# Performance work log

Measured on AMD Instinct MI355X. Metric: run time of the kernel, lower is better.

The kernel has to match this reference:

```python
import jax, jax.numpy as jnp
import numpy as np
import math

M, DIN, DTGT = 65536, 256, 256   # feature count and feature dims
S, SD_IN, SD_TGT = 64, 256, 256  # num_slots, in_slot_dim, tgt_slot_dim
ITERS = 3
H_IN = 128                        # mlp_in hidden (hardcoded 128 in source)
H_TGT = SD_TGT if SD_TGT > 128 else 128  # mlp_tgt hidden

ARGS = ["inputs", "target", "in_slots", "tgt_slots",
        "ln_in_g", "ln_in_b", "ln_tgt_g", "ln_tgt_b",
        "Wk", "bk", "Wv", "bv", "Wvt", "bvt",
        "ln_slots_g", "ln_slots_b", "Wq", "bq",
        "gru_in_Wih", "gru_in_Whh", "gru_in_bih", "gru_in_bhh",
        "gru_tgt_Wih", "gru_tgt_Whh", "gru_tgt_bih", "gru_tgt_bhh",
        "ln_mi_g", "ln_mi_b", "mi_W1", "mi_b1", "mi_W2", "mi_b2",
        "ln_mt_g", "ln_mt_b", "mt_W1", "mt_b1", "mt_W2", "mt_b2"]


def _ln(x, g, b):
    m = jnp.mean(x, axis=-1, keepdims=True)
    v = jnp.var(x, axis=-1, keepdims=True)
    return (x - m) * jax.lax.rsqrt(v + 1e-5) * g + b


def _gru(x, h, Wih, Whh, bih, bhh):
    # torch.nn.GRUCell semantics; Wih: (D, 3H), Whh: (H, 3H)
    H = h.shape[-1]
    gi = x @ Wih + bih
    gh = h @ Whh + bhh
    r = jax.nn.sigmoid(gi[:, :H] + gh[:, :H])
    z = jax.nn.sigmoid(gi[:, H:2 * H] + gh[:, H:2 * H])
    n = jnp.tanh(gi[:, 2 * H:] + r * gh[:, 2 * H:])
    return (1.0 - z) * n + z * h


def _forward(inputs, target, in_slots, tgt_slots,
             ln_in_g, ln_in_b, ln_tgt_g, ln_tgt_b,
             Wk, bk, Wv, bv, Wvt, bvt,
             ln_slots_g, ln_slots_b, Wq, bq,
             gru_in_Wih, gru_in_Whh, gru_in_bih, gru_in_bhh,
             gru_tgt_Wih, gru_tgt_Whh, gru_tgt_bih, gru_tgt_bhh,
             ln_mi_g, ln_mi_b, mi_W1, mi_b1, mi_W2, mi_b2,
             ln_mt_g, ln_mt_b, mt_W1, mt_b1, mt_W2, mt_b2):
    inputs_norm = _ln(inputs, ln_in_g, ln_in_b)          # [M, DIN]
    in_k = inputs_norm @ Wk + bk                          # [M, SD_IN]
    in_v = inputs_norm @ Wv + bv                          # [M, SD_IN]
    tgt_v = _ln(target, ln_tgt_g, ln_tgt_b) @ Wvt + bvt   # [M, SD_TGT]
    scale = 1.0 / math.sqrt(in_k.shape[1])
    attn = None
    for _ in range(ITERS):
        q = _ln(in_slots, ln_slots_g, ln_slots_b) @ Wq + bq   # [S, SD_IN]
        logits = (q @ in_k.T) * scale                          # [S, M]
        attn = jax.nn.softmax(logits, axis=0)                  # softmax over SLOTS (dim=0)
        in_up = attn @ in_v                                    # [S, SD_IN]
        tgt_up = attn @ tgt_v                                  # [S, SD_TGT]
        in_slots = _gru(in_up, in_slots, gru_in_Wih, gru_in_Whh, gru_in_bih, gru_in_bhh)
        tgt_slots = _gru(tgt_up, tgt_slots, gru_tgt_Wih, gru_tgt_Whh, gru_tgt_bih, gru_tgt_bhh)
        in_slots = in_slots + (jax.nn.relu(_ln(in_slots, ln_mi_g, ln_mi_b) @ mi_W1 + mi_b1) @ mi_W2 + mi_b2)
        tgt_slots = tgt_slots + (jax.nn.relu(_ln(tgt_slots, ln_mt_g, ln_mt_b) @ mt_W1 + mt_b1) @ mt_W2 + mt_b2)
    return (in_slots, tgt_slots, attn)


def setup_inputs() -> dict:
    key = jax.random.key(0)
    ks = iter(jax.random.split(key, 64))
    rn = lambda shape, s=1.0: jax.random.normal(next(ks), shape, dtype=jnp.float32) * s
    w = 0.02
    d = {
        "inputs": rn((M, DIN)),
        "target": rn((M, DTGT)),
        "in_slots": rn((S, SD_IN)),
        "tgt_slots": rn((S, SD_TGT)),
        "ln_in_g": jnp.ones((DIN,)), "ln_in_b": jnp.zeros((DIN,)),
        "ln_tgt_g": jnp.ones((DTGT,)), "ln_tgt_b": jnp.zeros((DTGT,)),
        "Wk": rn((DIN, SD_IN), w), "bk": jnp.zeros((SD_IN,)),
        "Wv": rn((DIN, SD_IN), w), "bv": jnp.zeros((SD_IN,)),
        "Wvt": rn((DTGT, SD_TGT), w), "bvt": jnp.zeros((SD_TGT,)),
        "ln_slots_g": jnp.ones((SD_IN,)), "ln_slots_b": jnp.zeros((SD_IN,)),
        "Wq": rn((SD_IN, SD_IN), w), "bq": jnp.zeros((SD_IN,)),
        "gru_in_Wih": rn((SD_IN, 3 * SD_IN), w), "gru_in_Whh": rn((SD_IN, 3 * SD_IN), w),
        "gru_in_bih": jnp.zeros((3 * SD_IN,)), "gru_in_bhh": jnp.zeros((3 * SD_IN,)),
        "gru_tgt_Wih": rn((SD_TGT, 3 * SD_TGT), w), "gru_tgt_Whh": rn((SD_TGT, 3 * SD_TGT), w),
        "gru_tgt_bih": jnp.zeros((3 * SD_TGT,)), "gru_tgt_bhh": jnp.zeros((3 * SD_TGT,)),
        "ln_mi_g": jnp.ones((SD_IN,)), "ln_mi_b": jnp.zeros((SD_IN,)),
        "mi_W1": rn((SD_IN, H_IN), w), "mi_b1": jnp.zeros((H_IN,)),
        "mi_W2": rn((H_IN, SD_IN), w), "mi_b2": jnp.zeros((SD_IN,)),
        "ln_mt_g": jnp.ones((SD_TGT,)), "ln_mt_b": jnp.zeros((SD_TGT,)),
        "mt_W1": rn((SD_TGT, H_TGT), w), "mt_b1": jnp.zeros((H_TGT,)),
        "mt_W2": rn((H_TGT, SD_TGT), w), "mt_b2": jnp.zeros((SD_TGT,)),
    }
    return {k: d[k] for k in ARGS}


def reference(inputs, target, in_slots, tgt_slots,
              ln_in_g, ln_in_b, ln_tgt_g, ln_tgt_b,
              Wk, bk, Wv, bv, Wvt, bvt,
              ln_slots_g, ln_slots_b, Wq, bq,
              gru_in_Wih, gru_in_Whh, gru_in_bih, gru_in_bhh,
              gru_tgt_Wih, gru_tgt_Whh, gru_tgt_bih, gru_tgt_bhh,
              ln_mi_g, ln_mi_b, mi_W1, mi_b1, mi_W2, mi_b2,
              ln_mt_g, ln_mt_b, mt_W1, mt_b1, mt_W2, mt_b2):
    return _forward(inputs, target, in_slots, tgt_slots,
                    ln_in_g, ln_in_b, ln_tgt_g, ln_tgt_b,
                    Wk, bk, Wv, bv, Wvt, bvt,
                    ln_slots_g, ln_slots_b, Wq, bq,
                    gru_in_Wih, gru_in_Whh, gru_in_bih, gru_in_bhh,
                    gru_tgt_Wih, gru_tgt_Whh, gru_tgt_bih, gru_tgt_bhh,
                    ln_mi_g, ln_mi_b, mi_W1, mi_b1, mi_W2, mi_b2,
                    ln_mt_g, ln_mt_b, mt_W1, mt_b1, mt_W2, mt_b2)
```

## Files before the change

### kernel.cpp

```cpp
#include <hip/hip_runtime.h>
#include <hip/hip_bf16.h>
#include <math.h>

typedef __bf16 bf16_t;
typedef __bf16 bf16x8 __attribute__((ext_vector_type(8)));
typedef __bf16 bf16x4 __attribute__((ext_vector_type(4)));
typedef float f32x4 __attribute__((ext_vector_type(4)));

#define DEVI __device__ __forceinline__

DEVI f32x4 mfma16(bf16x8 a, bf16x8 b, f32x4 c) {
  return __builtin_amdgcn_mfma_f32_16x16x32_bf16(a, b, c, 0, 0, 0);
}
DEVI bf16x8 ld8(const bf16_t* p) { return *reinterpret_cast<const bf16x8*>(p); }


struct WtArgs { const float* s0; const float* s1; const float* s2; const float* s3;
                const float* s4; const float* s5; const float* s6; const float* s7;
                const float* s8; const float* s9; const float* s10; const float* s11; };

__global__ __launch_bounds__(256) void k_wtrans(WtArgs A, bf16_t* __restrict__ wt) {
  constexpr int offs[12] = {0,65536,131072,196608,262144,458752,655360,851968,
                            1048576,1081344,1114112,1179648};
  constexpr int Ks[12]   = {256,256,256,256,256,256,256,256,256,128,256,256};
  constexpr int Ns[12]   = {256,256,256,256,768,768,768,768,128,256,256,256};
  const int m = blockIdx.y;
  const int K = Ks[m], N = Ns[m];
  const int tn = N >> 6;
  const int tile = blockIdx.x;
  if (tile >= (K >> 6) * tn) return;
  const int tk = tile / tn, tc = tile - tk * tn;
  const float* sp;
  switch (m) {
    case 0: sp = A.s0; break; case 1: sp = A.s1; break; case 2: sp = A.s2; break;
    case 3: sp = A.s3; break; case 4: sp = A.s4; break; case 5: sp = A.s5; break;
    case 6: sp = A.s6; break; case 7: sp = A.s7; break; case 8: sp = A.s8; break;
    case 9: sp = A.s9; break; case 10: sp = A.s10; break; default: sp = A.s11; break;
  }
  __shared__ float ts[64][65];
  const int t = threadIdx.x;
  const int k0 = tk * 64, n0 = tc * 64;
  {
    const int c = t & 63, rq = t >> 6;
    #pragma unroll
    for (int i = 0; i < 16; ++i) {
      const int r = rq * 16 + i;
      ts[r][c] = sp[(size_t)(k0 + r) * N + n0 + c];
    }
  }
  __syncthreads();
  bf16_t* dst = wt + offs[m];
  const int n_l = t & 63, kq = t >> 6;
  #pragma unroll
  for (int h = 0; h < 2; ++h) {
    const int k_l = kq * 16 + h * 8;
    bf16x8 pk;
    #pragma unroll
    for (int e = 0; e < 8; ++e) pk[e] = (bf16_t)ts[k_l + e][n_l];
    const int n_g = n0 + n_l, k_g = k0 + k_l;
    const int nt = n_g >> 4, kc = k_g >> 5;
    const int lane = (((k_g >> 3) & 3) << 4) + (n_g & 15);
    *reinterpret_cast<bf16x8*>(dst + (((size_t)(nt * (K >> 5) + kc)) << 9) + lane * 8) = pk;
  }
}

__global__ __launch_bounds__(256) void k_init(const float* __restrict__ in_slots,
                                              const float* __restrict__ tgt_slots,
                                              float* __restrict__ h_f32,
                                              bf16_t* __restrict__ h_bf) {
  int idx = blockIdx.x * 256 + threadIdx.x;
  int side = idx >> 14, j = idx & 16383;
  int s = j >> 8, d = j & 255;
  float x = (side ? tgt_slots : in_slots)[j];
  h_f32[idx] = x;
  h_bf[side*16384 + (((s>>4)*8 + (d>>5))<<9) + ((d>>3)&3)*128 + (s&15)*8 + (d&7)] = (bf16_t)x;
}

__global__ __launch_bounds__(256) void k_phaseA(
    const float* __restrict__ inputs, const float* __restrict__ target,
    const float* __restrict__ ln_in_g, const float* __restrict__ ln_in_b,
    const float* __restrict__ ln_tgt_g, const float* __restrict__ ln_tgt_b,
    const bf16_t* __restrict__ wkF, const bf16_t* __restrict__ wvF, const bf16_t* __restrict__ wvtF,
    const float* __restrict__ bk, const float* __restrict__ bv, const float* __restrict__ bvt,
    bf16_t* __restrict__ in_kF, bf16_t* __restrict__ in_vF, bf16_t* __restrict__ tgt_vF) {
  const int side = blockIdx.y;
  const int m0 = blockIdx.x * 64;
  const int t = threadIdx.x, l = t & 63, w = t >> 6;
  __shared__ __align__(16) bf16_t anorm[64][264];
  __shared__ __align__(16) bf16_t stg[4][64][68];
  const float* src = side ? target : inputs;
  const float* gp = side ? ln_tgt_g : ln_in_g;
  const float* bp = side ? ln_tgt_b : ln_in_b;
  const float4 g4 = *reinterpret_cast<const float4*>(gp + l * 4);
  const float4 b4 = *reinterpret_cast<const float4*>(bp + l * 4);
  float4 v[16];
  #pragma unroll
  for (int i = 0; i < 16; ++i)
    v[i] = *reinterpret_cast<const float4*>(src + (size_t)(m0 + w*16 + i) * 256 + l * 4);
  #pragma unroll
  for (int i = 0; i < 16; ++i) {
    float s1 = v[i].x + v[i].y + v[i].z + v[i].w;
    float s2 = v[i].x*v[i].x + v[i].y*v[i].y + v[i].z*v[i].z + v[i].w*v[i].w;
    #pragma unroll
    for (int msk = 1; msk < 64; msk <<= 1) { s1 += __shfl_xor(s1, msk); s2 += __shfl_xor(s2, msk); }
    const float mean = s1 * (1.f/256.f);
    const float rstd = rsqrtf(s2 * (1.f/256.f) - mean*mean + 1e-5f);
    bf16x4 pk;
    pk[0] = (bf16_t)((v[i].x - mean) * rstd * g4.x + b4.x);
    pk[1] = (bf16_t)((v[i].y - mean) * rstd * g4.y + b4.y);
    pk[2] = (bf16_t)((v[i].z - mean) * rstd * g4.z + b4.z);
    pk[3] = (bf16_t)((v[i].w - mean) * rstd * g4.w + b4.w);
    *reinterpret_cast<bf16x4*>(&anorm[w*16 + i][l*4]) = pk;
  }
  __syncthreads();
  const int l16 = l & 15, l4 = l >> 4;

  if (side == 0) {
    f32x4 acc[4][4] = {};
    for (int ks = 0; ks < 8; ++ks) {
      const int k = ks*32 + l4*8;
      bf16x8 a[4], b[4];
      #pragma unroll
      for (int mi = 0; mi < 4; ++mi) a[mi] = ld8(&anorm[mi*16 + l16][k]);
      #pragma unroll
      for (int ni = 0; ni < 4; ++ni) b[ni] = ld8(wkF + (((size_t)((w*4 + ni)*8 + ks)) << 9) + l*8);
      #pragma unroll
      for (int mi = 0; mi < 4; ++mi)
        #pragma unroll
        for (int ni = 0; ni < 4; ++ni) acc[mi][ni] = mfma16(a[mi], b[ni], acc[mi][ni]);
    }
    #pragma unroll
    for (int mi = 0; mi < 4; ++mi)
      #pragma unroll
      for (int ni = 0; ni < 4; ++ni) {
        const int d = w*64 + ni*16 + l16;
        const float bias = bk[d];
        #pragma unroll
        for (int rr = 0; rr < 4; ++rr)
          stg[w][mi*16 + l4*4 + rr][ni*16 + l16] = (bf16_t)(acc[mi][ni][rr] + bias);
      }
    #pragma unroll
    for (int mi = 0; mi < 4; ++mi)
      #pragma unroll
      for (int kc = 0; kc < 2; ++kc) {
        bf16x8 vv = *reinterpret_cast<const bf16x8*>(&stg[w][mi*16 + l16][kc*32 + l4*8]);
        *reinterpret_cast<bf16x8*>(in_kF +
            ((((size_t)(blockIdx.x*4 + mi))*8 + (w*2 + kc)) << 9) + l*8) = vv;
      }
  }
  {
    const bf16_t* WF = side ? wvtF : wvF;
    const float* bias = side ? bvt : bv;
    bf16_t* out = side ? tgt_vF : in_vF;
    f32x4 acc[4][4] = {};
    for (int ks = 0; ks < 8; ++ks) {
      const int k = ks*32 + l4*8;
      bf16x8 a[4], b[4];
      #pragma unroll
      for (int mi = 0; mi < 4; ++mi) a[mi] = ld8(WF + (((size_t)((w*4 + mi)*8 + ks)) << 9) + l*8);
      #pragma unroll
      for (int ni = 0; ni < 4; ++ni) b[ni] = ld8(&anorm[ni*16 + l16][k]);
      #pragma unroll
      for (int mi = 0; mi < 4; ++mi)
        #pragma unroll
        for (int ni = 0; ni < 4; ++ni) acc[mi][ni] = mfma16(a[mi], b[ni], acc[mi][ni]);
    }
    #pragma unroll
    for (int mi = 0; mi < 4; ++mi)
      #pragma unroll
      for (int ni = 0; ni < 4; ++ni)
        #pragma unroll
        for (int rr = 0; rr < 4; ++rr) {
          const int d = w*64 + mi*16 + l4*4 + rr;
          stg[w][mi*16 + l4*4 + rr][ni*16 + l16] = (bf16_t)(acc[mi][ni][rr] + bias[d]);
        }
    #pragma unroll
    for (int mi = 0; mi < 4; ++mi)
      #pragma unroll
      for (int mc = 0; mc < 2; ++mc) {
        bf16x8 vv = *reinterpret_cast<const bf16x8*>(&stg[w][mi*16 + l16][mc*32 + l4*8]);
        *reinterpret_cast<bf16x8*>(out +
            ((((size_t)(w*4 + mi))*2048 + (blockIdx.x*2 + mc)) << 9) + l*8) = vv;
      }
  }
}

__global__ __launch_bounds__(256) void k_q(
    const float* __restrict__ h_in,
    const float* __restrict__ ln_g, const float* __restrict__ ln_b,
    const bf16_t* __restrict__ wqF, const float* __restrict__ bq,
    bf16_t* __restrict__ q_bf) {
  __shared__ __align__(16) bf16_t anorm[64][264];
  const int t = threadIdx.x, l = t & 63, w = t >> 6;
  const float4 g4 = *reinterpret_cast<const float4*>(ln_g + l * 4);
  const float4 b4 = *reinterpret_cast<const float4*>(ln_b + l * 4);
  float4 v[16];
  #pragma unroll
  for (int i = 0; i < 16; ++i)
    v[i] = *reinterpret_cast<const float4*>(h_in + (size_t)(w*16 + i) * 256 + l * 4);
  #pragma unroll
  for (int i = 0; i < 16; ++i) {
    float s1 = v[i].x + v[i].y + v[i].z + v[i].w;
    float s2 = v[i].x*v[i].x + v[i].y*v[i].y + v[i].z*v[i].z + v[i].w*v[i].w;
    #pragma unroll
    for (int msk = 1; msk < 64; msk <<= 1) { s1 += __shfl_xor(s1, msk); s2 += __shfl_xor(s2, msk); }
    const float mean = s1 * (1.f/256.f);
    const float rstd = rsqrtf(s2 * (1.f/256.f) - mean*mean + 1e-5f);
    bf16x4 pk;
    pk[0] = (bf16_t)((v[i].x - mean) * rstd * g4.x + b4.x);
    pk[1] = (bf16_t)((v[i].y - mean) * rstd * g4.y + b4.y);
    pk[2] = (bf16_t)((v[i].z - mean) * rstd * g4.z + b4.z);
    pk[3] = (bf16_t)((v[i].w - mean) * rstd * g4.w + b4.w);
    *reinterpret_cast<bf16x4*>(&anorm[w*16 + i][l*4]) = pk;
  }
  __syncthreads();
  const int l16 = l & 15, l4 = l >> 4;
  f32x4 acc[4][4] = {};
  for (int ks = 0; ks < 8; ++ks) {
    const int k = ks*32 + l4*8;
    bf16x8 a[4], b[4];
    #pragma unroll
    for (int mi = 0; mi < 4; ++mi) a[mi] = ld8(&anorm[mi*16 + l16][k]);
    #pragma unroll
    for (int ni = 0; ni < 4; ++ni) b[ni] = ld8(wqF + (((size_t)((w*4 + ni)*8 + ks)) << 9) + l*8);
    #pragma unroll
    for (int mi = 0; mi < 4; ++mi)
      #pragma unroll
      for (int ni = 0; ni < 4; ++ni) acc[mi][ni] = mfma16(a[mi], b[ni], acc[mi][ni]);
  }
  #pragma unroll
  for (int mi = 0; mi < 4; ++mi)
    #pragma unroll
    for (int ni = 0; ni < 4; ++ni) {
      const int d = w*64 + ni*16 + l16;
      const float bias = bq[d];
      bf16_t* outp = q_bf + (((size_t)(mi*8 + w*2 + (ni>>1))) << 9) + ((ni&1)*2 + (l16>>3))*128 + (l16&7);
      #pragma unroll
      for (int rr = 0; rr < 4; ++rr)
        outp[(l4*4 + rr)*8] = (bf16_t)((acc[mi][ni][rr] + bias) * 0.0625f);
    }
}

__global__ __launch_bounds__(256) void k_logits(
    const bf16_t* __restrict__ q_bf, const bf16_t* __restrict__ in_kF,
    bf16_t* __restrict__ attnF, float* __restrict__ attn_f32, int write_f32) {
  __shared__ __align__(16) bf16_t stg[4][64][68];
  const int t = threadIdx.x, l = t & 63, w = t >> 6, l16 = l & 15, l4 = l >> 4;
  const int m0 = blockIdx.x * 256 + w * 64;
  f32x4 acc[4][4] = {};
  for (int ks = 0; ks < 8; ++ks) {
    bf16x8 a[4], b[4];
    #pragma unroll
    for (int mi = 0; mi < 4; ++mi) a[mi] = ld8(q_bf + (((size_t)(mi*8 + ks)) << 9) + l*8);
    #pragma unroll
    for (int ni = 0; ni < 4; ++ni)
      b[ni] = ld8(in_kF + (((size_t)((blockIdx.x*16 + w*4 + ni)*8 + ks)) << 9) + l*8);
    #pragma unroll
    for (int mi = 0; mi < 4; ++mi)
      #pragma unroll
      for (int ni = 0; ni < 4; ++ni) acc[mi][ni] = mfma16(a[mi], b[ni], acc[mi][ni]);
  }
  #pragma unroll
  for (int ni = 0; ni < 4; ++ni) {
    float mx = -3.0e38f;
    #pragma unroll
    for (int mi = 0; mi < 4; ++mi)
      #pragma unroll
      for (int rr = 0; rr < 4; ++rr) mx = fmaxf(mx, acc[mi][ni][rr]);
    mx = fmaxf(mx, __shfl_xor(mx, 16));
    mx = fmaxf(mx, __shfl_xor(mx, 32));
    float sm = 0.f;
    #pragma unroll
    for (int mi = 0; mi < 4; ++mi)
      #pragma unroll
      for (int rr = 0; rr < 4; ++rr) {
        float ev = __expf(acc[mi][ni][rr] - mx);
        acc[mi][ni][rr] = ev; sm += ev;
      }
    sm += __shfl_xor(sm, 16);
    sm += __shfl_xor(sm, 32);
    const float inv = 1.0f / sm;
    #pragma unroll
    for (int mi = 0; mi < 4; ++mi)
      #pragma unroll
      for (int rr = 0; rr < 4; ++rr) acc[mi][ni][rr] *= inv;
  }
  #pragma unroll
  for (int mi = 0; mi < 4; ++mi)
    #pragma unroll
    for (int ni = 0; ni < 4; ++ni)
      #pragma unroll
      for (int rr = 0; rr < 4; ++rr) {
        stg[w][mi*16 + l4*4 + rr][ni*16 + l16] = (bf16_t)acc[mi][ni][rr];
        if (write_f32) {
          const int s = mi*16 + l4*4 + rr;
          attn_f32[(size_t)s*65536 + (m0 + ni*16 + l16)] = acc[mi][ni][rr];
        }
      }
  #pragma unroll
  for (int mi = 0; mi < 4; ++mi)
    #pragma unroll
    for (int mc = 0; mc < 2; ++mc) {
      bf16x8 vv = *reinterpret_cast<const bf16x8*>(&stg[w][mi*16 + l16][mc*32 + l4*8]);
      *reinterpret_cast<bf16x8*>(attnF +
          ((((size_t)mi)*2048 + (blockIdx.x*8 + w*2 + mc)) << 9) + l*8) = vv;
    }
}

__global__ __launch_bounds__(256) void k_pv(
    const bf16_t* __restrict__ attnF,
    const bf16_t* __restrict__ in_vF, const bf16_t* __restrict__ tgt_vF,
    bf16_t* __restrict__ p_in, bf16_t* __restrict__ p_tgt) {
  const int c = blockIdx.x, side = blockIdx.y;
  const bf16_t* V = side ? tgt_vF : in_vF;
  bf16_t* P = side ? p_tgt : p_in;
  const int t = threadIdx.x, l = t & 63, w = t >> 6, l16 = l & 15, l4 = l >> 4;
  f32x4 acc[4][4] = {};
  for (int ks = 0; ks < 16; ++ks) {
    const size_t mc = c*16 + ks;
    bf16x8 a[4], b[4];
    #pragma unroll
    for (int mi = 0; mi < 4; ++mi) a[mi] = ld8(attnF + ((((size_t)mi)*2048 + mc) << 9) + l*8);
    #pragma unroll
    for (int ni = 0; ni < 4; ++ni) b[ni] = ld8(V + ((((size_t)(w*4 + ni))*2048 + mc) << 9) + l*8);
    #pragma unroll
    for (int mi = 0; mi < 4; ++mi)
      #pragma unroll
      for (int ni = 0; ni < 4; ++ni) acc[mi][ni] = mfma16(a[mi], b[ni], acc[mi][ni]);
  }
  #pragma unroll
  for (int mi = 0; mi < 4; ++mi)
    #pragma unroll
    for (int ni = 0; ni < 4; ++ni) {
      const int d = w*64 + ni*16 + l16;
      #pragma unroll
      for (int rr = 0; rr < 4; ++rr) {
        const int s = mi*16 + l4*4 + rr;
        P[(size_t)c*16384 + s*256 + d] = (bf16_t)acc[mi][ni][rr];
      }
    }
}

__global__ __launch_bounds__(256) void k_pvred(
    const bf16_t* __restrict__ p_in, const bf16_t* __restrict__ p_tgt,
    bf16_t* __restrict__ upF) {
  const int b = blockIdx.x;
  const int side = b >> 6, s = b & 63;
  const int d = threadIdx.x;
  const bf16_t* P = (side ? p_tgt : p_in) + s*256 + d;
  float sum = 0.f;
  #pragma unroll 8
  for (int cc = 0; cc < 128; ++cc) sum += (float)P[(size_t)cc * 16384];
  upF[side*16384 + (((s>>4)*8 + (d>>5))<<9) + ((d>>3)&3)*128 + (s&15)*8 + (d&7)] = (bf16_t)sum;
}

__global__ __launch_bounds__(256) void k_gates(
    const bf16_t* __restrict__ upF, const bf16_t* __restrict__ h_bf,
    const bf16_t* __restrict__ wihF_in, const bf16_t* __restrict__ whhF_in,
    const bf16_t* __restrict__ wihF_tgt, const bf16_t* __restrict__ whhF_tgt,
    const float* __restrict__ bih_in, const float* __restrict__ bhh_in,
    const float* __restrict__ bih_tgt, const float* __restrict__ bhh_tgt,
    float* __restrict__ gi, float* __restrict__ gh) {
  const int nchunk = blockIdx.x, which = blockIdx.y, side = blockIdx.z;
  const bf16_t* Aop = (which ? h_bf : upF) + side*16384;
  const bf16_t* WF = side ? (which ? whhF_tgt : wihF_tgt) : (which ? whhF_in : wihF_in);
  const float* bias = side ? (which ? bhh_tgt : bih_tgt) : (which ? bhh_in : bih_in);
  float* out = (which ? gh : gi) + side*49152;
  const int t = threadIdx.x, l = t & 63, w = t >> 6, l16 = l & 15, l4 = l >> 4;
  const int n0 = nchunk*256 + w*64;
  f32x4 acc[4][4] = {};
  for (int ks = 0; ks < 8; ++ks) {
    bf16x8 a[4], b[4];
    #pragma unroll
    for (int mi = 0; mi < 4; ++mi) a[mi] = ld8(Aop + (((size_t)(mi*8 + ks)) << 9) + l*8);
    #pragma unroll
    for (int ni = 0; ni < 4; ++ni)
      b[ni] = ld8(WF + (((size_t)((nchunk*16 + w*4 + ni)*8 + ks)) << 9) + l*8);
    #pragma unroll
    for (int mi = 0; mi < 4; ++mi)
      #pragma unroll
      for (int ni = 0; ni < 4; ++ni) acc[mi][ni] = mfma16(a[mi], b[ni], acc[mi][ni]);
  }
  #pragma unroll
  for (int mi = 0; mi < 4; ++mi)
    #pragma unroll
    for (int ni = 0; ni < 4; ++ni) {
      const int n = n0 + ni*16 + l16;
      const float bb = bias[n];
      #pragma unroll
      for (int rr = 0; rr < 4; ++rr) {
        const int s = mi*16 + l4*4 + rr;
        out[(size_t)s*768 + n] = acc[mi][ni][rr] + bb;
      }
    }
}

__global__ __launch_bounds__(256) void k_gru_ln(
    const float* __restrict__ gi, const float* __restrict__ gh,
    const float* __restrict__ h_f32,
    const float* __restrict__ ln_mi_g, const float* __restrict__ ln_mi_b,
    const float* __restrict__ ln_mt_g, const float* __restrict__ ln_mt_b,
    float* __restrict__ hp_f32, bf16_t* __restrict__ hpnF) {
  const int s = blockIdx.x, side = blockIdx.y;
  const int d = threadIdx.x;
  const float* GI = gi + side*49152 + s*768;
  const float* GH = gh + side*49152 + s*768;
  const float hv = h_f32[side*16384 + s*256 + d];
  const float rg = 1.f / (1.f + __expf(-(GI[d] + GH[d])));
  const float zg = 1.f / (1.f + __expf(-(GI[256 + d] + GH[256 + d])));
  const float ng = tanhf(GI[512 + d] + rg * GH[512 + d]);
  const float hp = (1.f - zg) * ng + zg * hv;
  float a = hp, b2 = hp * hp;
  #pragma unroll
  for (int msk = 1; msk < 64; msk <<= 1) { a += __shfl_xor(a, msk); b2 += __shfl_xor(b2, msk); }
  __shared__ float reda[4], redb[4];
  const int w = d >> 6, lid = d & 63;
  if (lid == 0) { reda[w] = a; redb[w] = b2; }
  __syncthreads();
  const float S1 = reda[0] + reda[1] + reda[2] + reda[3];
  const float S2 = redb[0] + redb[1] + redb[2] + redb[3];
  const float mean = S1 * (1.f/256.f);
  const float rstd = rsqrtf(S2 * (1.f/256.f) - mean*mean + 1e-5f);
  const float* g = side ? ln_mt_g : ln_mi_g;
  const float* bb = side ? ln_mt_b : ln_mi_b;
  const float nv = (hp - mean) * rstd * g[d] + bb[d];
  hp_f32[side*16384 + s*256 + d] = hp;
  hpnF[side*16384 + (((s>>4)*8 + (d>>5))<<9) + ((d>>3)&3)*128 + (s&15)*8 + (d&7)] = (bf16_t)nv;
}

__global__ __launch_bounds__(256) void k_mlpq(
    const bf16_t* __restrict__ hpnF,
    const bf16_t* __restrict__ w1F_in, const bf16_t* __restrict__ w1F_tgt,
    const float* __restrict__ b1_in, const float* __restrict__ b1_tgt,
    const bf16_t* __restrict__ w2F_in, const bf16_t* __restrict__ w2F_tgt,
    const float* __restrict__ b2_in, const float* __restrict__ b2_tgt,
    const float* __restrict__ hp_f32,
    float* __restrict__ h_f32, bf16_t* __restrict__ h_bf, float* __restrict__ slots_out,
    const float* __restrict__ ln_sg, const float* __restrict__ ln_sb,
    const bf16_t* __restrict__ wqF, const float* __restrict__ bq,
    bf16_t* __restrict__ q_bf, int make_q) {
  const int side = blockIdx.x;
  __shared__ __align__(16) bf16_t hid[64][264];
  const int t = threadIdx.x, l = t & 63, w = t >> 6, l16 = l & 15, l4 = l >> 4;
  const int NH = side ? 256 : 128;
  {
    const bf16_t* Aop = hpnF + side*16384;
    const bf16_t* WF = side ? w1F_tgt : w1F_in;
    const float* b1 = side ? b1_tgt : b1_in;
    const int ntiles = NH >> 6;
    for (int nt = 0; nt < ntiles; ++nt) {
      const int n0 = w*(NH>>2) + nt*16;
      f32x4 acc[4] = {};
      for (int ks = 0; ks < 8; ++ks) {
        bf16x8 b = ld8(WF + (((size_t)((n0>>4)*8 + ks)) << 9) + l*8);
        #pragma unroll
        for (int mt = 0; mt < 4; ++mt)
          acc[mt] = mfma16(ld8(Aop + (((size_t)(mt*8 + ks)) << 9) + l*8), b, acc[mt]);
      }
      const float bb = b1[n0 + l16];
      #pragma unroll
      for (int mt = 0; mt < 4; ++mt)
        #pragma unroll
        for (int rr = 0; rr < 4; ++rr) {
          const int s = mt*16 + l4*4 + rr;
          hid[s][n0 + l16] = (bf16_t)fmaxf(acc[mt][rr] + bb, 0.f);
        }
    }
  }
  __syncthreads();
  {
    const bf16_t* WF = side ? w2F_tgt : w2F_in;
    const float* b2 = side ? b2_tgt : b2_in;
    const int ksteps = NH >> 5;
    #pragma unroll
    for (int nt = 0; nt < 4; ++nt) {
      const int n0 = w*64 + nt*16;
      f32x4 acc[4] = {};
      for (int ks = 0; ks < ksteps; ++ks) {
        const int k = ks*32 + l4*8;
        bf16x8 b = ld8(WF + (((size_t)((n0>>4)*ksteps + ks)) << 9) + l*8);
        #pragma unroll
        for (int mt = 0; mt < 4; ++mt)
          acc[mt] = mfma16(ld8(&hid[mt*16 + l16][k]), b, acc[mt]);
      }
      const int n = n0 + l16;
      const float bb = b2[n];
      #pragma unroll
      for (int mt = 0; mt < 4; ++mt)
        #pragma unroll
        for (int rr = 0; rr < 4; ++rr) {
          const int s = mt*16 + l4*4 + rr;
          const int idx = side*16384 + s*256 + n;
          const float val = acc[mt][rr] + bb + hp_f32[idx];
          h_f32[idx] = val;
          slots_out[idx] = val;
          h_bf[side*16384 + (((s>>4)*8 + (n>>5))<<9) + ((n>>3)&3)*128 + (s&15)*8 + (n&7)] = (bf16_t)val;
        }
    }
  }
  if (!make_q || side != 0) return;
  __syncthreads();
  {
    for (int i = 0; i < 16; ++i) {
      const int s = w*16 + i;
      float4 x = *reinterpret_cast<const float4*>(h_f32 + s*256 + 4*l);
      float a = x.x + x.y + x.z + x.w;
      float b2s = x.x*x.x + x.y*x.y + x.z*x.z + x.w*x.w;
      #pragma unroll
      for (int msk = 1; msk < 64; msk <<= 1) { a += __shfl_xor(a, msk); b2s += __shfl_xor(b2s, msk); }
      const float mean = a * (1.f/256.f);
      const float rstd = rsqrtf(b2s * (1.f/256.f) - mean*mean + 1e-5f);
      float4 g4 = *reinterpret_cast<const float4*>(ln_sg + 4*l);
      float4 bb4 = *reinterpret_cast<const float4*>(ln_sb + 4*l);
      bf16x4 pk;
      pk[0] = (bf16_t)((x.x - mean) * rstd * g4.x + bb4.x);
      pk[1] = (bf16_t)((x.y - mean) * rstd * g4.y + bb4.y);
      pk[2] = (bf16_t)((x.z - mean) * rstd * g4.z + bb4.z);
      pk[3] = (bf16_t)((x.w - mean) * rstd * g4.w + bb4.w);
      *reinterpret_cast<bf16x4*>(&hid[s][4*l]) = pk;
    }
  }
  __syncthreads();
  {
    #pragma unroll
    for (int nt = 0; nt < 4; ++nt) {
      const int n0 = w*64 + nt*16;
      f32x4 acc[4] = {};
      for (int ks = 0; ks < 8; ++ks) {
        const int k = ks*32 + l4*8;
        bf16x8 b = ld8(wqF + (((size_t)((n0>>4)*8 + ks)) << 9) + l*8);
        #pragma unroll
        for (int mt = 0; mt < 4; ++mt)
          acc[mt] = mfma16(ld8(&hid[mt*16 + l16][k]), b, acc[mt]);
      }
      const int d = n0 + l16;
      const float bb = bq[d];
      #pragma unroll
      for (int mt = 0; mt < 4; ++mt) {
        bf16_t* op = q_bf + (((size_t)(mt*8 + (d>>5))) << 9) + ((d>>3)&3)*128 + (d&7);
        #pragma unroll
        for (int rr = 0; rr < 4; ++rr)
          op[(l4*4 + rr)*8] = (bf16_t)((acc[mt][rr] + bb) * 0.0625f);
      }
    }
  }
}

extern "C" void kernel_launch(void* const* d_in, const int* in_sizes, int n_in,
                              void* d_out, int out_size, void* d_ws, size_t ws_size,
                              hipStream_t stream) {
  (void)in_sizes; (void)n_in; (void)out_size; (void)ws_size;
  const float* inputs     = (const float*)d_in[0];
  const float* target     = (const float*)d_in[1];
  const float* in_slots   = (const float*)d_in[2];
  const float* tgt_slots  = (const float*)d_in[3];
  const float* ln_in_g    = (const float*)d_in[4];
  const float* ln_in_b    = (const float*)d_in[5];
  const float* ln_tgt_g   = (const float*)d_in[6];
  const float* ln_tgt_b   = (const float*)d_in[7];
  const float* Wk  = (const float*)d_in[8];
  const float* bk  = (const float*)d_in[9];
  const float* Wv  = (const float*)d_in[10];
  const float* bv  = (const float*)d_in[11];
  const float* Wvt = (const float*)d_in[12];
  const float* bvt = (const float*)d_in[13];
  const float* ln_slots_g = (const float*)d_in[14];
  const float* ln_slots_b = (const float*)d_in[15];
  const float* Wq  = (const float*)d_in[16];
  const float* bq  = (const float*)d_in[17];
  const float* gru_in_Wih  = (const float*)d_in[18];
  const float* gru_in_Whh  = (const float*)d_in[19];
  const float* gru_in_bih  = (const float*)d_in[20];
  const float* gru_in_bhh  = (const float*)d_in[21];
  const float* gru_tgt_Wih = (const float*)d_in[22];
  const float* gru_tgt_Whh = (const float*)d_in[23];
  const float* gru_tgt_bih = (const float*)d_in[24];
  const float* gru_tgt_bhh = (const float*)d_in[25];
  const float* ln_mi_g = (const float*)d_in[26];
  const float* ln_mi_b = (const float*)d_in[27];
  const float* mi_W1 = (const float*)d_in[28];
  const float* mi_b1 = (const float*)d_in[29];
  const float* mi_W2 = (const float*)d_in[30];
  const float* mi_b2 = (const float*)d_in[31];
  const float* ln_mt_g = (const float*)d_in[32];
  const float* ln_mt_b = (const float*)d_in[33];
  const float* mt_W1 = (const float*)d_in[34];
  const float* mt_b1 = (const float*)d_in[35];
  const float* mt_W2 = (const float*)d_in[36];
  const float* mt_b2 = (const float*)d_in[37];

  char* ws = (char*)d_ws;
  bf16_t* wt      = (bf16_t*)(ws);
  bf16_t* in_kF   = (bf16_t*)(ws + 2490368ull);
  bf16_t* in_vF   = (bf16_t*)(ws + 36044800ull);
  bf16_t* tgt_vF  = (bf16_t*)(ws + 69599232ull);
  bf16_t* attnF   = (bf16_t*)(ws + 103153664ull);
  bf16_t* q_bf    = (bf16_t*)(ws + 111542272ull);
  bf16_t* h_bf    = (bf16_t*)(ws + 111575040ull);
  bf16_t* upF     = (bf16_t*)(ws + 111640576ull);
  bf16_t* hpnF    = (bf16_t*)(ws + 111673344ull);
  float*  h_f32   = (float*)(ws + 111706112ull);
  float*  hp_f32  = (float*)(ws + 111837184ull);
  float*  gi      = (float*)(ws + 111968256ull);
  float*  gh      = (float*)(ws + 112361472ull);
  bf16_t* p_in    = (bf16_t*)(ws + 112754688ull);
  bf16_t* p_tgt   = (bf16_t*)(ws + 116948992ull);

  bf16_t* wkF = wt;
  bf16_t* wvF = wt + 65536;
  bf16_t* wvtF = wt + 131072;
  bf16_t* wqF = wt + 196608;
  bf16_t* wihF_in  = wt + 262144;
  bf16_t* whhF_in  = wt + 458752;
  bf16_t* wihF_tgt = wt + 655360;
  bf16_t* whhF_tgt = wt + 851968;
  bf16_t* w1F_in  = wt + 1048576;
  bf16_t* w2F_in  = wt + 1081344;
  bf16_t* w1F_tgt = wt + 1114112;
  bf16_t* w2F_tgt = wt + 1179648;

  float* attn_out = (float*)d_out + 32768;

  WtArgs wa = {Wk, Wv, Wvt, Wq, gru_in_Wih, gru_in_Whh, gru_tgt_Wih, gru_tgt_Whh,
               mi_W1, mi_W2, mt_W1, mt_W2};
  k_wtrans<<<dim3(48, 12), 256, 0, stream>>>(wa, wt);
  k_init<<<128, 256, 0, stream>>>(in_slots, tgt_slots, h_f32, h_bf);
  k_phaseA<<<dim3(1024, 2), 256, 0, stream>>>(inputs, target, ln_in_g, ln_in_b,
      ln_tgt_g, ln_tgt_b, wkF, wvF, wvtF, bk, bv, bvt, in_kF, in_vF, tgt_vF);
  k_q<<<1, 256, 0, stream>>>(h_f32, ln_slots_g, ln_slots_b, wqF, bq, q_bf);

  for (int it = 0; it < 3; ++it) {
    k_logits<<<256, 256, 0, stream>>>(q_bf, in_kF, attnF, attn_out, it == 2 ? 1 : 0);
    k_pv<<<dim3(128, 2), 256, 0, stream>>>(attnF, in_vF, tgt_vF, p_in, p_tgt);
    k_pvred<<<128, 256, 0, stream>>>(p_in, p_tgt, upF);
    k_gates<<<dim3(3, 2, 2), 256, 0, stream>>>(upF, h_bf, wihF_in, whhF_in,
        wihF_tgt, whhF_tgt, gru_in_bih, gru_in_bhh, gru_tgt_bih, gru_tgt_bhh, gi, gh);
    k_gru_ln<<<dim3(64, 2), 256, 0, stream>>>(gi, gh, h_f32, ln_mi_g, ln_mi_b,
        ln_mt_g, ln_mt_b, hp_f32, hpnF);
    k_mlpq<<<2, 256, 0, stream>>>(hpnF, w1F_in, w1F_tgt, mi_b1, mt_b1,
        w2F_in, w2F_tgt, mi_b2, mt_b2, hp_f32, h_f32, h_bf, (float*)d_out,
        ln_slots_g, ln_slots_b, wqF, bq, q_bf, it < 2 ? 1 : 0);
  }
}
```

Before: 313.3 us.

## Fold LayerNorm affine into projection weights and store GEMM outputs directly

The LayerNorm gamma is folded into Wk/Wv/Wvt during weight transposition, and a new small kernel folds beta into the projection biases. In the projection kernel, inputs are loaded directly into the MFMA fragment layout with a shorter per-row reduction, and the LDS staging buffer is removed so outputs are written straight to global memory in the tiled layout. This cuts LDS traffic and per-element affine work in the large input-projection kernel, at the cost of scattered narrow global stores, one extra launch, and a small rounding difference from folding gamma before the bf16 cast.

```diff
diff --git a/kernel.cpp b/kernel.cpp
--- a/kernel.cpp
+++ b/kernel.cpp
@@ -19,7 +19,9 @@
                 const float* s4; const float* s5; const float* s6; const float* s7;
                 const float* s8; const float* s9; const float* s10; const float* s11; };
 
-__global__ __launch_bounds__(256) void k_wtrans(WtArgs A, bf16_t* __restrict__ wt) {
+__global__ __launch_bounds__(256) void k_wtrans(WtArgs A, bf16_t* __restrict__ wt,
+                                                const float* __restrict__ g_in,
+                                                const float* __restrict__ g_tgt) {
   constexpr int offs[12] = {0,65536,131072,196608,262144,458752,655360,851968,
                             1048576,1081344,1114112,1179648};
   constexpr int Ks[12]   = {256,256,256,256,256,256,256,256,256,128,256,256};
@@ -37,6 +39,7 @@
     case 6: sp = A.s6; break; case 7: sp = A.s7; break; case 8: sp = A.s8; break;
     case 9: sp = A.s9; break; case 10: sp = A.s10; break; default: sp = A.s11; break;
   }
+  const float* gv = (m == 2) ? g_tgt : ((m < 2) ? g_in : nullptr);
   __shared__ float ts[64][65];
   const int t = threadIdx.x;
   const int k0 = tk * 64, n0 = tc * 64;
@@ -45,7 +48,9 @@
     #pragma unroll
     for (int i = 0; i < 16; ++i) {
       const int r = rq * 16 + i;
-      ts[r][c] = sp[(size_t)(k0 + r) * N + n0 + c];
+      float val = sp[(size_t)(k0 + r) * N + n0 + c];
+      if (gv) val *= gv[k0 + r];
+      ts[r][c] = val;
     }
   }
   __syncthreads();
@@ -62,6 +67,21 @@
     const int lane = (((k_g >> 3) & 3) << 4) + (n_g & 15);
     *reinterpret_cast<bf16x8*>(dst + (((size_t)(nt * (K >> 5) + kc)) << 9) + lane * 8) = pk;
   }
+}
+
+__global__ __launch_bounds__(256) void k_bias(
+    const float* __restrict__ Wk, const float* __restrict__ Wv, const float* __restrict__ Wvt,
+    const float* __restrict__ b_in, const float* __restrict__ b_tgt,
+    const float* __restrict__ bk, const float* __restrict__ bv, const float* __restrict__ bvt,
+    float* __restrict__ out) {
+  const int which = blockIdx.x;
+  const float* W = which == 0 ? Wk : (which == 1 ? Wv : Wvt);
+  const float* bvec = which == 2 ? b_tgt : b_in;
+  const float* bias = which == 0 ? bk : (which == 1 ? bv : bvt);
+  const int n = threadIdx.x;
+  float sum = bias[n];
+  for (int k = 0; k < 256; ++k) sum += bvec[k] * W[(size_t)k * 256 + n];
+  out[which * 256 + n] = sum;
 }
 
 __global__ __launch_bounds__(256) void k_init(const float* __restrict__ in_slots,
@@ -76,112 +96,124 @@
   h_bf[side*16384 + (((s>>4)*8 + (d>>5))<<9) + ((d>>3)&3)*128 + (s&15)*8 + (d&7)] = (bf16_t)x;
 }
 
+DEVI void gemm_pass(const bf16_t* aFl, const bf16_t* __restrict__ WF,
+                    int w, int l, f32x4 acc[4][4]) {
+  #pragma unroll 1
+  for (int ks = 0; ks < 8; ++ks) {
+    bf16x8 a[4], b[4];
+    #pragma unroll
+    for (int mt = 0; mt < 4; ++mt) a[mt] = ld8(aFl + ((mt*8 + ks) << 9) + l*8);
+    #pragma unroll
+    for (int dt = 0; dt < 4; ++dt) b[dt] = ld8(WF + (((size_t)((w*4 + dt)*8 + ks)) << 9) + l*8);
+    #pragma unroll
+    for (int mt = 0; mt < 4; ++mt)
+      #pragma unroll
+      for (int dt = 0; dt < 4; ++dt) acc[mt][dt] = mfma16(a[mt], b[dt], acc[mt][dt]);
+  }
+}
+
 __global__ __launch_bounds__(256) void k_phaseA(
     const float* __restrict__ inputs, const float* __restrict__ target,
-    const float* __restrict__ ln_in_g, const float* __restrict__ ln_in_b,
-    const float* __restrict__ ln_tgt_g, const float* __restrict__ ln_tgt_b,
     const bf16_t* __restrict__ wkF, const bf16_t* __restrict__ wvF, const bf16_t* __restrict__ wvtF,
-    const float* __restrict__ bk, const float* __restrict__ bv, const float* __restrict__ bvt,
+    const float* __restrict__ bfold,
     bf16_t* __restrict__ in_kF, bf16_t* __restrict__ in_vF, bf16_t* __restrict__ tgt_vF) {
   const int side = blockIdx.y;
   const int m0 = blockIdx.x * 64;
   const int t = threadIdx.x, l = t & 63, w = t >> 6;
-  __shared__ __align__(16) bf16_t anorm[64][264];
-  __shared__ __align__(16) bf16_t stg[4][64][68];
-  const float* src = side ? target : inputs;
-  const float* gp = side ? ln_tgt_g : ln_in_g;
-  const float* bp = side ? ln_tgt_b : ln_in_b;
-  const float4 g4 = *reinterpret_cast<const float4*>(gp + l * 4);
-  const float4 b4 = *reinterpret_cast<const float4*>(bp + l * 4);
-  float4 v[16];
-  #pragma unroll
-  for (int i = 0; i < 16; ++i)
-    v[i] = *reinterpret_cast<const float4*>(src + (size_t)(m0 + w*16 + i) * 256 + l * 4);
-  #pragma unroll
-  for (int i = 0; i < 16; ++i) {
-    float s1 = v[i].x + v[i].y + v[i].z + v[i].w;
-    float s2 = v[i].x*v[i].x + v[i].y*v[i].y + v[i].z*v[i].z + v[i].w*v[i].w;
-    #pragma unroll
-    for (int msk = 1; msk < 64; msk <<= 1) { s1 += __shfl_xor(s1, msk); s2 += __shfl_xor(s2, msk); }
+  const int l16 = l & 15, l4 = l >> 4;
+  __shared__ __align__(16) bf16_t aF[16384];
+
+  {
+    const float* src = side ? target : inputs;
+    const int row = m0 + w*16 + l16;
+    const float* srcp = src + (size_t)row * 256 + l4 * 8;
+    float4 xa[8], xb[8];
+    #pragma unroll
+    for (int j = 0; j < 8; ++j) {
+      xa[j] = *reinterpret_cast<const float4*>(srcp + j*32);
+      xb[j] = *reinterpret_cast<const float4*>(srcp + j*32 + 4);
+    }
+    float s1 = 0.f, s2 = 0.f;
+    #pragma unroll
+    for (int j = 0; j < 8; ++j) {
+      s1 += xa[j].x + xa[j].y + xa[j].z + xa[j].w + xb[j].x + xb[j].y + xb[j].z + xb[j].w;
+      s2 += xa[j].x*xa[j].x + xa[j].y*xa[j].y + xa[j].z*xa[j].z + xa[j].w*xa[j].w
+          + xb[j].x*xb[j].x + xb[j].y*xb[j].y + xb[j].z*xb[j].z + xb[j].w*xb[j].w;
+    }
+    s1 += __shfl_xor(s1, 16); s1 += __shfl_xor(s1, 32);
+    s2 += __shfl_xor(s2, 16); s2 += __shfl_xor(s2, 32);
     const float mean = s1 * (1.f/256.f);
     const float rstd = rsqrtf(s2 * (1.f/256.f) - mean*mean + 1e-5f);
-    bf16x4 pk;
-    pk[0] = (bf16_t)((v[i].x - mean) * rstd * g4.x + b4.x);
-    pk[1] = (bf16_t)((v[i].y - mean) * rstd * g4.y + b4.y);
-    pk[2] = (bf16_t)((v[i].z - mean) * rstd * g4.z + b4.z);
-    pk[3] = (bf16_t)((v[i].w - mean) * rstd * g4.w + b4.w);
-    *reinterpret_cast<bf16x4*>(&anorm[w*16 + i][l*4]) = pk;
+    #pragma unroll
+    for (int j = 0; j < 8; ++j) {
+      bf16x8 pk;
+      pk[0] = (bf16_t)((xa[j].x - mean) * rstd);
+      pk[1] = (bf16_t)((xa[j].y - mean) * rstd);
+      pk[2] = (bf16_t)((xa[j].z - mean) * rstd);
+      pk[3] = (bf16_t)((xa[j].w - mean) * rstd);
+      pk[4] = (bf16_t)((xb[j].x - mean) * rstd);
+      pk[5] = (bf16_t)((xb[j].y - mean) * rstd);
+      pk[6] = (bf16_t)((xb[j].z - mean) * rstd);
+      pk[7] = (bf16_t)((xb[j].w - mean) * rstd);
+      *reinterpret_cast<bf16x8*>(aF + ((w*8 + j) << 9) + l*8) = pk;
+    }
   }
   __syncthreads();
-  const int l16 = l & 15, l4 = l >> 4;
 
   if (side == 0) {
+    {
+      f32x4 acc[4][4] = {};
+      gemm_pass(aF, wkF, w, l, acc);
+      #pragma unroll
+      for (int mt = 0; mt < 4; ++mt) {
+        const int mtg = blockIdx.x*4 + mt;
+        #pragma unroll
+        for (int dt = 0; dt < 4; ++dt) {
+          const int dtg = w*4 + dt;
+          const float bias = bfold[dtg*16 + l16];
+          bf16_t* bp = in_kF + (((size_t)(mtg*8 + (dtg>>1))) << 9)
+                       + ((dtg&1)*2 + (l16>>3))*128 + (l16&7);
+          #pragma unroll
+          for (int rr = 0; rr < 4; ++rr)
+            bp[(l4*4 + rr)*8] = (bf16_t)(acc[mt][dt][rr] + bias);
+        }
+      }
+    }
+    {
+      f32x4 acc[4][4] = {};
+      gemm_pass(aF, wvF, w, l, acc);
+      #pragma unroll
+      for (int mt = 0; mt < 4; ++mt) {
+        const int mcg = blockIdx.x*2 + (mt>>1);
+        #pragma unroll
+        for (int dt = 0; dt < 4; ++dt) {
+          const int dtg = w*4 + dt;
+          const float bias = bfold[256 + dtg*16 + l16];
+          bf16x4 pk;
+          #pragma unroll
+          for (int rr = 0; rr < 4; ++rr) pk[rr] = (bf16_t)(acc[mt][dt][rr] + bias);
+          *reinterpret_cast<bf16x4*>(in_vF + (((size_t)(dtg*2048 + mcg)) << 9)
+              + ((mt&1)*2 + (l4>>1))*128 + l16*8 + (l4&1)*4) = pk;
+        }
+      }
+    }
+  } else {
     f32x4 acc[4][4] = {};
-    for (int ks = 0; ks < 8; ++ks) {
-      const int k = ks*32 + l4*8;
-      bf16x8 a[4], b[4];
-      #pragma unroll
-      for (int mi = 0; mi < 4; ++mi) a[mi] = ld8(&anorm[mi*16 + l16][k]);
-      #pragma unroll
-      for (int ni = 0; ni < 4; ++ni) b[ni] = ld8(wkF + (((size_t)((w*4 + ni)*8 + ks)) << 9) + l*8);
-      #pragma unroll
-      for (int mi = 0; mi < 4; ++mi)
-        #pragma unroll
-        for (int ni = 0; ni < 4; ++ni) acc[mi][ni] = mfma16(a[mi], b[ni], acc[mi][ni]);
-    }
-    #pragma unroll
-    for (int mi = 0; mi < 4; ++mi)
-      #pragma unroll
-      for (int ni = 0; ni < 4; ++ni) {
-        const int d = w*64 + ni*16 + l16;
-        const float bias = bk[d];
-        #pragma unroll
-        for (int rr = 0; rr < 4; ++rr)
-          stg[w][mi*16 + l4*4 + rr][ni*16 + l16] = (bf16_t)(acc[mi][ni][rr] + bias);
-      }
-    #pragma unroll
-    for (int mi = 0; mi < 4; ++mi)
-      #pragma unroll
-      for (int kc = 0; kc < 2; ++kc) {
-        bf16x8 vv = *reinterpret_cast<const bf16x8*>(&stg[w][mi*16 + l16][kc*32 + l4*8]);
-        *reinterpret_cast<bf16x8*>(in_kF +
-            ((((size_t)(blockIdx.x*4 + mi))*8 + (w*2 + kc)) << 9) + l*8) = vv;
-      }
-  }
-  {
-    const bf16_t* WF = side ? wvtF : wvF;
-    const float* bias = side ? bvt : bv;
-    bf16_t* out = side ? tgt_vF : in_vF;
-    f32x4 acc[4][4] = {};
-    for (int ks = 0; ks < 8; ++ks) {
-      const int k = ks*32 + l4*8;
-      bf16x8 a[4], b[4];
-      #pragma unroll
-      for (int mi = 0; mi < 4; ++mi) a[mi] = ld8(WF + (((size_t)((w*4 + mi)*8 + ks)) << 9) + l*8);
-      #pragma unroll
-      for (int ni = 0; ni < 4; ++ni) b[ni] = ld8(&anorm[ni*16 + l16][k]);
-      #pragma unroll
-      for (int mi = 0; mi < 4; ++mi)
-        #pragma unroll
-        for (int ni = 0; ni < 4; ++ni) acc[mi][ni] = mfma16(a[mi], b[ni], acc[mi][ni]);
-    }
-    #pragma unroll
-    for (int mi = 0; mi < 4; ++mi)
-      #pragma unroll
-      for (int ni = 0; ni < 4; ++ni)
-        #pragma unroll
-        for (int rr = 0; rr < 4; ++rr) {
-          const int d = w*64 + mi*16 + l4*4 + rr;
-          stg[w][mi*16 + l4*4 + rr][ni*16 + l16] = (bf16_t)(acc[mi][ni][rr] + bias[d]);
-        }
-    #pragma unroll
-    for (int mi = 0; mi < 4; ++mi)
-      #pragma unroll
-      for (int mc = 0; mc < 2; ++mc) {
-        bf16x8 vv = *reinterpret_cast<const bf16x8*>(&stg[w][mi*16 + l16][mc*32 + l4*8]);
-        *reinterpret_cast<bf16x8*>(out +
-            ((((size_t)(w*4 + mi))*2048 + (blockIdx.x*2 + mc)) << 9) + l*8) = vv;
-      }
+    gemm_pass(aF, wvtF, w, l, acc);
+    #pragma unroll
+    for (int mt = 0; mt < 4; ++mt) {
+      const int mcg = blockIdx.x*2 + (mt>>1);
+      #pragma unroll
+      for (int dt = 0; dt < 4; ++dt) {
+        const int dtg = w*4 + dt;
+        const float bias = bfold[512 + dtg*16 + l16];
+        bf16x4 pk;
+        #pragma unroll
+        for (int rr = 0; rr < 4; ++rr) pk[rr] = (bf16_t)(acc[mt][dt][rr] + bias);
+        *reinterpret_cast<bf16x4*>(tgt_vF + (((size_t)(dtg*2048 + mcg)) << 9)
+            + ((mt&1)*2 + (l4>>1))*128 + l16*8 + (l4&1)*4) = pk;
+      }
+    }
   }
 }
 
@@ -605,6 +637,7 @@
   float*  gh      = (float*)(ws + 112361472ull);
   bf16_t* p_in    = (bf16_t*)(ws + 112754688ull);
   bf16_t* p_tgt   = (bf16_t*)(ws + 116948992ull);
+  float*  bfold   = (float*)(ws + 121143296ull);
 
   bf16_t* wkF = wt;
   bf16_t* wvF = wt + 65536;
@@ -623,10 +656,11 @@
 
   WtArgs wa = {Wk, Wv, Wvt, Wq, gru_in_Wih, gru_in_Whh, gru_tgt_Wih, gru_tgt_Whh,
                mi_W1, mi_W2, mt_W1, mt_W2};
-  k_wtrans<<<dim3(48, 12), 256, 0, stream>>>(wa, wt);
+  k_wtrans<<<dim3(48, 12), 256, 0, stream>>>(wa, wt, ln_in_g, ln_tgt_g);
+  k_bias<<<3, 256, 0, stream>>>(Wk, Wv, Wvt, ln_in_b, ln_tgt_b, bk, bv, bvt, bfold);
   k_init<<<128, 256, 0, stream>>>(in_slots, tgt_slots, h_f32, h_bf);
-  k_phaseA<<<dim3(1024, 2), 256, 0, stream>>>(inputs, target, ln_in_g, ln_in_b,
-      ln_tgt_g, ln_tgt_b, wkF, wvF, wvtF, bk, bv, bvt, in_kF, in_vF, tgt_vF);
+  k_phaseA<<<dim3(1024, 2), 256, 0, stream>>>(inputs, target,
+      wkF, wvF, wvtF, bfold, in_kF, in_vF, tgt_vF);
   k_q<<<1, 256, 0, stream>>>(h_f32, ln_slots_g, ln_slots_b, wqF, bq, q_bf);
 
   for (int it = 0; it < 3; ++it) {
```

Result: slower. 322.6 us (+3.0%).
